# Kernel optimization log

Measured on AMD Instinct MI355X. Metric: run time of the kernel, lower is better.

## Reference

```python
import jax, jax.numpy as jnp
import numpy as np

B, H, D = 2, 16, 64
M = N = 4096
WM = WN = 64
R = 3
NEG = -10000.0


def _rand_blocks(m, n, wm, wn, r, last_idx):
    # Faithful port of bigbird_block_rand_mask (numpy RNG, seeded by caller).
    nb = m // wm
    rand = np.zeros((nb - 2, r), dtype=np.int32)
    mid = np.arange(1, n // wn - 1, dtype=np.int32)
    last = n // wn - 1
    if last_idx > 2 * wn:
        last = last_idx // wn - 1
    for i in range(1, nb - 1):
        start, end = i - 2, i
        if i == 1:
            rand[i - 1] = np.random.permutation(mid[2:last])[:r]
        elif i == 2:
            rand[i - 1] = np.random.permutation(mid[3:last])[:r]
        elif i == nb - 3 or i == nb - 2:
            rand[i - 1] = np.random.permutation(mid[:last])[:r]
        elif start > last:
            rand[i - 1] = np.random.permutation(mid[:last])[:r]
        elif end + 1 == last:
            rand[i - 1] = np.random.permutation(mid[:start])[:r]
        else:
            rand[i - 1] = np.random.permutation(np.concatenate((mid[:start], mid[end + 1:last])))[:r]
    return rand


def setup_inputs() -> dict:
    key = jax.random.key(0)
    kq, kk, kv = jax.random.split(key, 3)
    nb = M // WM
    q = jax.random.normal(kq, (B, H, M, D), jnp.float32)
    k = jax.random.normal(kk, (B, H, N, D), jnp.float32)
    v = jax.random.normal(kv, (B, H, N, D), jnp.float32)
    band_mask = jnp.ones((B, 1, nb - 4, WM, 3 * WN), jnp.float32)
    from_mask = jnp.ones((B, 1, M, 1), jnp.float32)
    to_mask = jnp.ones((B, 1, 1, N), jnp.float32)
    from_blocked_mask = jnp.ones((B, nb, WM), jnp.float32)
    to_blocked_mask = jnp.ones((B, nb, WN), jnp.float32)
    np.random.seed(0)
    ra = np.stack([_rand_blocks(M, N, WM, WN, R, 1024)[:nb - 2] for _ in range(H)], 0)
    rand_attn = jnp.asarray(np.broadcast_to(ra[None], (B, H, nb - 2, R)).copy(), jnp.int32)
    return dict(query_layer=q, key_layer=k, value_layer=v, band_mask=band_mask,
                from_mask=from_mask, to_mask=to_mask,
                from_blocked_mask=from_blocked_mask, to_blocked_mask=to_blocked_mask,
                rand_attn=rand_attn, batch_size=B, from_seq_length=M, to_seq_length=N)


def _forward(q, k, v, band_mask, from_mask, to_mask, from_blocked_mask, to_blocked_mask, rand_attn):
    b, h, m, d = q.shape
    n = k.shape[2]
    wm, wn, r = WM, WN, R
    nb = m // wm
    scale = 1.0 / np.sqrt(d)
    bq = q.reshape(b, h, nb, wm, d)
    bk = k.reshape(b, h, nb, wn, d)
    bv = v.reshape(b, h, nb, wn, d)

    # gather random key/value blocks: [b,h,nb-2,r*wn,d]
    idx = jnp.broadcast_to(rand_attn.reshape(b, h, (nb - 2) * r, 1, 1).astype(jnp.int32),
                           (b, h, (nb - 2) * r, wn, d))
    gk = jnp.take_along_axis(bk, idx, axis=2).reshape(b, h, nb - 2, r * wn, d)
    gv = jnp.take_along_axis(bv, idx, axis=2).reshape(b, h, nb - 2, r * wn, d)

    # random-block attention mask: [b,h,nb-2,wm,r*wn]
    bidx = jnp.arange(b)[:, None, None, None]
    rm = to_blocked_mask[bidx, rand_attn].reshape(b, h, nb - 2, r * wn)
    rand_mask = jnp.einsum('blq,bhlk->bhlqk', from_blocked_mask[:, 1:-1], rm)

    # --- first row-block: full attention over all keys ---
    p0 = jnp.einsum('bhqd,bhkd->bhqk', bq[:, :, 0], k) * scale + (1.0 - to_mask) * NEG
    c0 = jnp.einsum('bhqk,bhkd->bhqd', jax.nn.softmax(p0, -1), v)[:, :, None]

    # --- second row-block: blocks 0,1,2,last + random ---
    k1c = jnp.concatenate([bk[:, :, 0], bk[:, :, 1], bk[:, :, 2], bk[:, :, -1], gk[:, :, 0]], axis=2)
    v1c = jnp.concatenate([bv[:, :, 0], bv[:, :, 1], bv[:, :, 2], bv[:, :, -1], gv[:, :, 0]], axis=2)
    p1 = jnp.einsum('bhqd,bhkd->bhqk', bq[:, :, 1], k1c) * scale
    seq_pad = jnp.concatenate([to_mask[:, :, :, :3 * wn], to_mask[:, :, :, -wn:],
                               jnp.ones((b, 1, 1, r * wn), to_mask.dtype)], axis=3)
    rpad = jnp.concatenate([jnp.ones((b, h, wm, 4 * wn), rand_mask.dtype), rand_mask[:, :, 0]], axis=3)
    p1 = p1 + (1.0 - jnp.minimum(seq_pad, rpad)) * NEG
    c1 = jnp.einsum('bhqk,bhkd->bhqd', jax.nn.softmax(p1, -1), v1c)[:, :, None]

    # --- middle row-blocks: sliding window (3 blocks) + first + last + random ---
    ek = jnp.concatenate([bk[:, :, 1:-3], bk[:, :, 2:-2], bk[:, :, 3:-1]], axis=3)  # [b,h,nb-4,3wn,d]
    ev = jnp.concatenate([bv[:, :, 1:-3], bv[:, :, 2:-2], bv[:, :, 3:-1]], axis=3)
    mq = bq[:, :, 2:-2]
    inner = jnp.einsum('bhlqd,bhlkd->bhlqk', mq, ek) * scale + (1.0 - band_mask) * NEG
    randp = jnp.einsum('bhlqd,bhlkd->bhlqk', mq, gk[:, :, 1:-1]) * scale + (1.0 - rand_mask[:, :, 1:-1]) * NEG
    firstp = jnp.einsum('bhlqd,bhkd->bhlqk', mq, bk[:, :, 0]) * scale \
        + (1.0 - to_mask[:, :, :, :wn][:, :, :, None, :]) * NEG
    lastp = jnp.einsum('bhlqd,bhkd->bhlqk', mq, bk[:, :, -1]) * scale \
        + (1.0 - to_mask[:, :, :, -wn:][:, :, :, None, :]) * NEG
    band = jnp.concatenate([firstp, inner, randp, lastp], axis=-1)  # [b,h,nb-4,wm,(5+r)*wn]
    attn = jax.nn.softmax(band, -1)
    cmid = (jnp.einsum('bhlqk,bhlkd->bhlqd', attn[..., wn:4 * wn], ev)
            + jnp.einsum('bhlqk,bhlkd->bhlqd', attn[..., 4 * wn:4 * wn + r * wn], gv[:, :, 1:-1])
            + jnp.einsum('bhlqk,bhkd->bhlqd', attn[..., :wn], bv[:, :, 0])
            + jnp.einsum('bhlqk,bhkd->bhlqd', attn[..., -wn:], bv[:, :, -1]))

    # --- second-to-last row-block: blocks 0,-3,-2,-1 + random ---
    k2c = jnp.concatenate([bk[:, :, 0], bk[:, :, -3], bk[:, :, -2], bk[:, :, -1], gk[:, :, -1]], axis=2)
    v2c = jnp.concatenate([bv[:, :, 0], bv[:, :, -3], bv[:, :, -2], bv[:, :, -1], gv[:, :, -1]], axis=2)
    p2 = jnp.einsum('bhqd,bhkd->bhqk', bq[:, :, -2], k2c) * scale
    seq_pad2 = jnp.concatenate([to_mask[:, :, :, :wn], to_mask[:, :, :, -3 * wn:],
                                jnp.ones((b, 1, 1, r * wn), to_mask.dtype)], axis=3)
    rpad2 = jnp.concatenate([jnp.ones((b, h, wm, 4 * wn), rand_mask.dtype), rand_mask[:, :, -1]], axis=3)
    p2 = p2 + (1.0 - jnp.minimum(seq_pad2, rpad2)) * NEG
    c2 = jnp.einsum('bhqk,bhkd->bhqd', jax.nn.softmax(p2, -1), v2c)[:, :, None]

    # --- last row-block: full attention ---
    p3 = jnp.einsum('bhqd,bhkd->bhqk', bq[:, :, -1], k) * scale + (1.0 - to_mask) * NEG
    c3 = jnp.einsum('bhqk,bhkd->bhqd', jax.nn.softmax(p3, -1), v)[:, :, None]

    ctx = jnp.concatenate([c0, c1, cmid, c2, c3], axis=2).reshape(b, h, m, d) * from_mask
    return jnp.transpose(ctx, (0, 2, 1, 3))  # [b, m, h, d]


def reference(query_layer, key_layer, value_layer, band_mask, from_mask, to_mask,
              from_blocked_mask, to_blocked_mask, rand_attn,
              batch_size, from_seq_length, to_seq_length):
    return _forward(query_layer, key_layer, value_layer, band_mask, from_mask, to_mask,
                    from_blocked_mask, to_blocked_mask, rand_attn)
```

## Files before the change

### kernel.cpp

```cpp
#include <hip/hip_runtime.h>
#include <math.h>

constexpr int B_  = 2;
constexpr int H_  = 16;
constexpr int M_  = 4096;
constexpr int NB_ = 64;
constexpr int R_  = 3;
constexpr float LOG2E  = 1.44269504089f;
constexpr float SCALE2 = 0.125f * LOG2E;
constexpr float NEG2   = -10000.0f * LOG2E;

constexpr int PER_BH = 62 + 16;
constexpr int NWG    = B_ * H_ * PER_BH;
constexpr int PACC_OFF = 0;
constexpr int PM_OFF   = B_ * H_ * 2 * 8 * 64 * 64;
constexpr int PL_OFF   = PM_OFF + B_ * H_ * 2 * 8 * 64;

typedef short bf16x8 __attribute__((ext_vector_type(8)));
typedef float f32x4  __attribute__((ext_vector_type(4)));

__device__ __forceinline__ short bf16s(float x) {
    return __builtin_bit_cast(short, (__bf16)x);
}
__device__ __forceinline__ unsigned pack_bf16(float a, float b) {
    unsigned short ul = __builtin_bit_cast(unsigned short, (__bf16)a);
    unsigned short uh = __builtin_bit_cast(unsigned short, (__bf16)b);
    return (unsigned)ul | ((unsigned)uh << 16);
}

__device__ __forceinline__ int tile_kb(int e, int ch, int qb, int ra0, int ra1, int ra2, int i) {
    if (e >= 0) return ch * 8 + i;
    const int rnd = (i == 4) ? ra0 : ((i == 5) ? ra1 : ra2);
    if (qb == 1)        return (i < 3) ? i : ((i == 3) ? NB_ - 1 : rnd);
    if (qb == NB_ - 2)  return (i == 0) ? 0 : ((i < 4) ? 60 + i : rnd);
    if (i == 0) return 0;
    if (i < 4)  return qb - 2 + i;
    if (i < 7)  return rnd;
    return NB_ - 1;
}

__global__ __launch_bounds__(256, 4)
void bigbird_mfma(const float* __restrict__ q,  const float* __restrict__ k,
                  const float* __restrict__ v,  const float* __restrict__ band_mask,
                  const float* __restrict__ from_mask, const float* __restrict__ to_mask,
                  const float* __restrict__ from_blocked, const float* __restrict__ to_blocked,
                  const int*   __restrict__ rand_attn,   float* __restrict__ out,
                  float* __restrict__ ws)
{
    __shared__ int4 kf[2][8][64];
    __shared__ int4 vf[2][8][64];

    const int wg  = (blockIdx.x & 7) * (NWG / 8) + (blockIdx.x >> 3);
    const int bh  = wg / PER_BH;
    const int idx = wg % PER_BH;
    const int h   = bh % H_;
    const int b   = bh / H_;
    int qb, e = -1, ch = 0;
    if (idx < 62)      { qb = idx + 1; }
    else if (idx < 70) { e = 0; ch = idx - 62; qb = 0; }
    else               { e = 1; ch = idx - 70; qb = NB_ - 1; }

    const int t  = threadIdx.x;
    const int l  = t & 63;
    const int w  = t >> 6;
    const int c  = l & 15;
    const int hh = l >> 4;

    int ra0 = 0, ra1 = 0, ra2 = 0;
    int nkb;
    if (e >= 0) nkb = 8;
    else {
        const int* ra = rand_attn + ((b * H_ + h) * (NB_ - 2) + (qb - 1)) * R_;
        ra0 = ra[0]; ra1 = ra[1]; ra2 = ra[2];
        nkb = (qb == 1 || qb == NB_ - 2) ? 7 : 8;
    }

    const int rr  = t >> 2;
    const int cc4 = t & 3;
    const float* kbase = k + ((size_t)bh * M_ + rr) * 64 + cc4 * 16;
    const int kslot = (rr >> 4) * 2 + (cc4 >> 1);
    const int kr15  = rr & 15;
    const int kg0   = (cc4 & 1) * 2;

    const int d0v  = (t & 31) * 2;
    const int oct8 = t >> 5;
    const float* vbase = v + (size_t)bh * M_ * 64 + (size_t)(oct8 * 8) * 64 + d0v;
    const int vslot = (d0v >> 4) * 2 + (oct8 >> 2);
    const int vidx  = (oct8 & 3) * 16 + (d0v & 15);

    bf16x8 qf[2];
    {
        const float* qp = q + ((size_t)bh * M_ + (size_t)qb * 64 + w * 16 + c) * 64 + hh * 8;
        #pragma unroll
        for (int dh = 0; dh < 2; ++dh) {
            float4 a0 = *(const float4*)(qp + dh * 32);
            float4 a1 = *(const float4*)(qp + dh * 32 + 4);
            bf16x8 qv;
            qv[0] = bf16s(a0.x); qv[1] = bf16s(a0.y); qv[2] = bf16s(a0.z); qv[3] = bf16s(a0.w);
            qv[4] = bf16s(a1.x); qv[5] = bf16s(a1.y); qv[6] = bf16s(a1.z); qv[7] = bf16s(a1.w);
            qf[dh] = qv;
        }
    }

    const float fbv = from_blocked[(b * NB_ + qb) * 64 + (w * 16 + c)];

    float mrun = -INFINITY, lrun = 0.0f;
    f32x4 O[4];
    #pragma unroll
    for (int nf = 0; nf < 4; ++nf) { O[nf][0] = 0.f; O[nf][1] = 0.f; O[nf][2] = 0.f; O[nf][3] = 0.f; }

    float4 kr0, kr1, kr2, kr3;
    float2 vr[8];

    {
        const int kb0 = tile_kb(e, ch, qb, ra0, ra1, ra2, 0);
        const float4* kp4 = (const float4*)(kbase + (size_t)kb0 * 4096);
        kr0 = kp4[0]; kr1 = kp4[1]; kr2 = kp4[2]; kr3 = kp4[3];
        const float* vp = vbase + (size_t)kb0 * 4096;
        #pragma unroll
        for (int j = 0; j < 8; ++j) vr[j] = *(const float2*)(vp + j * 64);

        float kfl[16];
        kfl[0]=kr0.x; kfl[1]=kr0.y; kfl[2]=kr0.z; kfl[3]=kr0.w;
        kfl[4]=kr1.x; kfl[5]=kr1.y; kfl[6]=kr1.z; kfl[7]=kr1.w;
        kfl[8]=kr2.x; kfl[9]=kr2.y; kfl[10]=kr2.z; kfl[11]=kr2.w;
        kfl[12]=kr3.x; kfl[13]=kr3.y; kfl[14]=kr3.z; kfl[15]=kr3.w;
        bf16x8 o0, o1;
        #pragma unroll
        for (int j = 0; j < 8; ++j) { o0[j] = bf16s(kfl[j]); o1[j] = bf16s(kfl[8 + j]); }
        kf[0][kslot][kg0 * 16 + kr15]       = __builtin_bit_cast(int4, o0);
        kf[0][kslot][(kg0 + 1) * 16 + kr15] = __builtin_bit_cast(int4, o1);

        bf16x8 va, vb2;
        #pragma unroll
        for (int j = 0; j < 8; ++j) { va[j] = bf16s(vr[j].x); vb2[j] = bf16s(vr[j].y); }
        vf[0][vslot][vidx]     = __builtin_bit_cast(int4, va);
        vf[0][vslot][vidx + 1] = __builtin_bit_cast(int4, vb2);

        if (1 < nkb) {
            const int kb1 = tile_kb(e, ch, qb, ra0, ra1, ra2, 1);
            const float4* kn4 = (const float4*)(kbase + (size_t)kb1 * 4096);
            kr0 = kn4[0]; kr1 = kn4[1]; kr2 = kn4[2]; kr3 = kn4[3];
            const float* vn = vbase + (size_t)kb1 * 4096;
            #pragma unroll
            for (int j = 0; j < 8; ++j) vr[j] = *(const float2*)(vn + j * 64);
        }
    }
    __syncthreads();

    for (int it = 0; it < nkb; ++it) {
        const int cur = it & 1;
        const int kb = tile_kb(e, ch, qb, ra0, ra1, ra2, it);
        int mode = 0, boff = 0;
        if (e < 0) {
            if (qb == 1 || qb == NB_ - 2) { mode = (it >= 4) ? 2 : 0; }
            else {
                if (it >= 1 && it < 4)      { mode = 1; boff = (it - 1) * 64; }
                else if (it >= 4 && it < 7) { mode = 2; }
            }
        }

        f32x4 sf[4];
        #pragma unroll
        for (int f = 0; f < 4; ++f) { sf[f][0]=0.f; sf[f][1]=0.f; sf[f][2]=0.f; sf[f][3]=0.f; }
        __builtin_amdgcn_s_setprio(1);
        #pragma unroll
        for (int f = 0; f < 4; ++f) {
            sf[f] = __builtin_amdgcn_mfma_f32_16x16x32_bf16(
                        __builtin_bit_cast(bf16x8, kf[cur][f * 2 + 0][l]), qf[0], sf[f], 0, 0, 0);
            sf[f] = __builtin_amdgcn_mfma_f32_16x16x32_bf16(
                        __builtin_bit_cast(bf16x8, kf[cur][f * 2 + 1][l]), qf[1], sf[f], 0, 0, 0);
        }
        __builtin_amdgcn_s_setprio(0);

        float msk[4][4];
        if (mode == 0) {
            const float* mp = to_mask + b * M_ + kb * 64 + 4 * hh;
            #pragma unroll
            for (int f = 0; f < 4; ++f) {
                float4 mv = *(const float4*)(mp + 16 * f);
                msk[f][0] = mv.x; msk[f][1] = mv.y; msk[f][2] = mv.z; msk[f][3] = mv.w;
            }
        } else if (mode == 1) {
            const float* mp = band_mask + (((size_t)b * (NB_ - 4) + (qb - 2)) * 64 + (w * 16 + c)) * 192 + boff + 4 * hh;
            #pragma unroll
            for (int f = 0; f < 4; ++f) {
                float4 mv = *(const float4*)(mp + 16 * f);
                msk[f][0] = mv.x; msk[f][1] = mv.y; msk[f][2] = mv.z; msk[f][3] = mv.w;
            }
        } else {
            const float* mp = to_blocked + (b * NB_ + kb) * 64 + 4 * hh;
            #pragma unroll
            for (int f = 0; f < 4; ++f) {
                float4 mv = *(const float4*)(mp + 16 * f);
                msk[f][0] = fbv * mv.x; msk[f][1] = fbv * mv.y;
                msk[f][2] = fbv * mv.z; msk[f][3] = fbv * mv.w;
            }
        }

        float p[4][4];
        float tmax = -INFINITY;
        #pragma unroll
        for (int f = 0; f < 4; ++f) {
            #pragma unroll
            for (int r = 0; r < 4; ++r) {
                const float s = sf[f][r] * SCALE2 + (1.0f - msk[f][r]) * NEG2;
                p[f][r] = s;
                tmax = fmaxf(tmax, s);
            }
        }
        tmax = fmaxf(tmax, __shfl_xor(tmax, 16));
        tmax = fmaxf(tmax, __shfl_xor(tmax, 32));
        const float mnew = fmaxf(mrun, tmax);
        const float fs = exp2f(mrun - mnew);
        float sum = 0.0f;
        #pragma unroll
        for (int f = 0; f < 4; ++f) {
            #pragma unroll
            for (int r = 0; r < 4; ++r) { p[f][r] = exp2f(p[f][r] - mnew); sum += p[f][r]; }
        }
        sum += __shfl_xor(sum, 16);
        sum += __shfl_xor(sum, 32);
        lrun = lrun * fs + sum;
        mrun = mnew;

        const float fr0 = __shfl(fs, hh * 4 + 0);
        const float fr1 = __shfl(fs, hh * 4 + 1);
        const float fr2 = __shfl(fs, hh * 4 + 2);
        const float fr3 = __shfl(fs, hh * 4 + 3);
        #pragma unroll
        for (int nf = 0; nf < 4; ++nf) {
            O[nf][0] *= fr0; O[nf][1] *= fr1; O[nf][2] *= fr2; O[nf][3] *= fr3;
        }

        unsigned pks[4][2];
        #pragma unroll
        for (int f = 0; f < 4; ++f) {
            pks[f][0] = pack_bf16(p[f][0], p[f][1]);
            pks[f][1] = pack_bf16(p[f][2], p[f][3]);
        }
        #pragma unroll
        for (int kh = 0; kh < 2; ++kh) {
            unsigned ad[4];
            #pragma unroll
            for (int wq = 0; wq < 4; ++wq) {
                const int pos = wq >> 1, ww = wq & 1;
                const int src = c + 16 * ((2 * hh + pos) & 3);
                const unsigned x = (unsigned)__shfl((int)pks[2 * kh][ww], src);
                const unsigned y = (unsigned)__shfl((int)pks[2 * kh + 1][ww], src);
                ad[wq] = (hh & 2) ? y : x;
            }
            const uint4 adv = make_uint4(ad[0], ad[1], ad[2], ad[3]);
            const bf16x8 pa = __builtin_bit_cast(bf16x8, adv);
            __builtin_amdgcn_s_setprio(1);
            #pragma unroll
            for (int nf = 0; nf < 4; ++nf) {
                O[nf] = __builtin_amdgcn_mfma_f32_16x16x32_bf16(
                            pa, __builtin_bit_cast(bf16x8, vf[cur][nf * 2 + kh][l]), O[nf], 0, 0, 0);
            }
            __builtin_amdgcn_s_setprio(0);
        }

        if (it + 1 < nkb) {
            const int nxt = cur ^ 1;
            float kfl[16];
            kfl[0]=kr0.x; kfl[1]=kr0.y; kfl[2]=kr0.z; kfl[3]=kr0.w;
            kfl[4]=kr1.x; kfl[5]=kr1.y; kfl[6]=kr1.z; kfl[7]=kr1.w;
            kfl[8]=kr2.x; kfl[9]=kr2.y; kfl[10]=kr2.z; kfl[11]=kr2.w;
            kfl[12]=kr3.x; kfl[13]=kr3.y; kfl[14]=kr3.z; kfl[15]=kr3.w;
            bf16x8 o0, o1;
            #pragma unroll
            for (int j = 0; j < 8; ++j) { o0[j] = bf16s(kfl[j]); o1[j] = bf16s(kfl[8 + j]); }
            kf[nxt][kslot][kg0 * 16 + kr15]       = __builtin_bit_cast(int4, o0);
            kf[nxt][kslot][(kg0 + 1) * 16 + kr15] = __builtin_bit_cast(int4, o1);

            bf16x8 va, vb2;
            #pragma unroll
            for (int j = 0; j < 8; ++j) { va[j] = bf16s(vr[j].x); vb2[j] = bf16s(vr[j].y); }
            vf[nxt][vslot][vidx]     = __builtin_bit_cast(int4, va);
            vf[nxt][vslot][vidx + 1] = __builtin_bit_cast(int4, vb2);

            if (it + 2 < nkb) {
                const int kbn = tile_kb(e, ch, qb, ra0, ra1, ra2, it + 2);
                const float4* kp4 = (const float4*)(kbase + (size_t)kbn * 4096);
                kr0 = kp4[0]; kr1 = kp4[1]; kr2 = kp4[2]; kr3 = kp4[3];
                const float* vp = vbase + (size_t)kbn * 4096;
                #pragma unroll
                for (int j = 0; j < 8; ++j) vr[j] = *(const float2*)(vp + j * 64);
            }
        }
        __syncthreads();
    }

    if (e < 0) {
        #pragma unroll
        for (int r = 0; r < 4; ++r) {
            const float lr  = __shfl(lrun, hh * 4 + r);
            const int   qg  = qb * 64 + w * 16 + hh * 4 + r;
            const float fmv = from_mask[b * M_ + qg];
            const float scl = fmv / lr;
            float* op = out + (((size_t)b * M_ + qg) * H_ + h) * 64 + c;
            #pragma unroll
            for (int nf = 0; nf < 4; ++nf) op[nf * 16] = O[nf][r] * scl;
        }
    } else {
        const int pe = (bh * 2 + e) * 8 + ch;
        #pragma unroll
        for (int r = 0; r < 4; ++r) {
            const int qlocal = w * 16 + hh * 4 + r;
            float* pa = ws + PACC_OFF + ((size_t)pe * 64 + qlocal) * 64 + c;
            #pragma unroll
            for (int nf = 0; nf < 4; ++nf) pa[nf * 16] = O[nf][r];
        }
        if (hh == 0) {
            ws[PM_OFF + pe * 64 + w * 16 + c] = mrun;
            ws[PL_OFF + pe * 64 + w * 16 + c] = lrun;
        }
    }
}

__global__ __launch_bounds__(256)
void bigbird_combine(const float* __restrict__ ws, const float* __restrict__ from_mask,
                     float* __restrict__ out)
{
    const int g  = blockIdx.x;
    const int e  = g & 1;
    const int bh = g >> 1;
    const int h  = bh % H_;
    const int b  = bh / H_;
    const int qb = e ? NB_ - 1 : 0;

    const int t  = threadIdx.x;
    const int r  = t >> 2;
    const int dq = (t & 3) * 16;

    float mc[8], lc[8];
    float m = -INFINITY;
    #pragma unroll
    for (int c = 0; c < 8; ++c) {
        mc[c] = ws[PM_OFF + (g * 8 + c) * 64 + r];
        lc[c] = ws[PL_OFF + (g * 8 + c) * 64 + r];
        m = fmaxf(m, mc[c]);
    }
    float l = 0.0f;
    float acc[16];
    #pragma unroll
    for (int j = 0; j < 16; ++j) acc[j] = 0.0f;
    #pragma unroll
    for (int c = 0; c < 8; ++c) {
        const float sc = exp2f(mc[c] - m);
        l += lc[c] * sc;
        const float4* pa = (const float4*)(ws + PACC_OFF + ((size_t)(g * 8 + c) * 64 + r) * 64 + dq);
        #pragma unroll
        for (int j4 = 0; j4 < 4; ++j4) {
            float4 av = pa[j4];
            acc[j4 * 4 + 0] += sc * av.x;
            acc[j4 * 4 + 1] += sc * av.y;
            acc[j4 * 4 + 2] += sc * av.z;
            acc[j4 * 4 + 3] += sc * av.w;
        }
    }
    const float fm = from_mask[b * M_ + qb * 64 + r];
    const float s  = fm / l;
    float* op = out + (((size_t)b * M_ + qb * 64 + r) * H_ + h) * 64 + dq;
    #pragma unroll
    for (int j4 = 0; j4 < 4; ++j4) {
        float4 o;
        o.x = acc[j4 * 4 + 0] * s; o.y = acc[j4 * 4 + 1] * s;
        o.z = acc[j4 * 4 + 2] * s; o.w = acc[j4 * 4 + 3] * s;
        *(float4*)(op + j4 * 4) = o;
    }
}

extern "C" void kernel_launch(void* const* d_in, const int* in_sizes, int n_in,
                              void* d_out, int out_size, void* d_ws, size_t ws_size,
                              hipStream_t stream) {
    const float* q  = (const float*)d_in[0];
    const float* k  = (const float*)d_in[1];
    const float* v  = (const float*)d_in[2];
    const float* bm = (const float*)d_in[3];
    const float* fm = (const float*)d_in[4];
    const float* tm = (const float*)d_in[5];
    const float* fb = (const float*)d_in[6];
    const float* tb = (const float*)d_in[7];
    const int*   ra = (const int*)d_in[8];
    float* o  = (float*)d_out;
    float* ws = (float*)d_ws;

    hipLaunchKernelGGL(bigbird_mfma, dim3(NWG), dim3(256), 0, stream,
                       q, k, v, bm, fm, tm, fb, tb, ra, o, ws);
    hipLaunchKernelGGL(bigbird_combine, dim3(B_ * H_ * 2), dim3(256), 0, stream,
                       ws, fm, o);
}
```

Measured before the change: 92.43 us.

## Prefetch masks one tile ahead, stage next K/V earlier, lighten barriers

```diff
diff --git a/kernel.cpp b/kernel.cpp
--- a/kernel.cpp
+++ b/kernel.cpp
@@ -26,6 +26,12 @@
     unsigned short ul = __builtin_bit_cast(unsigned short, (__bf16)a);
     unsigned short uh = __builtin_bit_cast(unsigned short, (__bf16)b);
     return (unsigned)ul | ((unsigned)uh << 16);
+}
+
+__device__ __forceinline__ void lds_barrier() {
+    asm volatile("s_waitcnt lgkmcnt(0)" ::: "memory");
+    __builtin_amdgcn_s_barrier();
+    asm volatile("" ::: "memory");
 }
 
 __device__ __forceinline__ int tile_kb(int e, int ch, int qb, int ra0, int ra1, int ra2, int i) {
@@ -37,6 +43,15 @@
     if (i < 4)  return qb - 2 + i;
     if (i < 7)  return rnd;
     return NB_ - 1;
+}
+
+__device__ __forceinline__ int tile_mode(int e, int qb, int i, int& boff) {
+    boff = 0;
+    if (e >= 0) return 0;
+    if (qb == 1 || qb == NB_ - 2) return (i >= 4) ? 2 : 0;
+    if (i >= 1 && i < 4) { boff = (i - 1) * 64; return 1; }
+    if (i >= 4 && i < 7) return 2;
+    return 0;
 }
 
 __global__ __launch_bounds__(256, 4)
@@ -88,6 +103,12 @@
     const int vslot = (d0v >> 4) * 2 + (oct8 >> 2);
     const int vidx  = (oct8 & 3) * 16 + (d0v & 15);
 
+    auto mask_ptr = [&](int kb, int mode, int boff) -> const float* {
+        if (mode == 0) return to_mask + b * M_ + kb * 64 + 4 * hh;
+        if (mode == 1) return band_mask + (((size_t)b * (NB_ - 4) + (qb - 2)) * 64 + (w * 16 + c)) * 192 + boff + 4 * hh;
+        return to_blocked + (b * NB_ + kb) * 64 + 4 * hh;
+    };
+
     bf16x8 qf[2];
     {
         const float* qp = q + ((size_t)bh * M_ + (size_t)qb * 64 + w * 16 + c) * 64 + hh * 8;
@@ -111,6 +132,7 @@
 
     float4 kr0, kr1, kr2, kr3;
     float2 vr[8];
+    float4 mpf[4];
 
     {
         const int kb0 = tile_kb(e, ch, qb, ra0, ra1, ra2, 0);
@@ -137,6 +159,11 @@
         vf[0][vslot][vidx]     = __builtin_bit_cast(int4, va);
         vf[0][vslot][vidx + 1] = __builtin_bit_cast(int4, vb2);
 
+        int bo0; const int md0 = tile_mode(e, qb, 0, bo0);
+        const float* mp = mask_ptr(kb0, md0, bo0);
+        #pragma unroll
+        for (int f = 0; f < 4; ++f) mpf[f] = *(const float4*)(mp + 16 * f);
+
         if (1 < nkb) {
             const int kb1 = tile_kb(e, ch, qb, ra0, ra1, ra2, 1);
             const float4* kn4 = (const float4*)(kbase + (size_t)kb1 * 4096);
@@ -146,19 +173,11 @@
             for (int j = 0; j < 8; ++j) vr[j] = *(const float2*)(vn + j * 64);
         }
     }
-    __syncthreads();
+    lds_barrier();
 
     for (int it = 0; it < nkb; ++it) {
         const int cur = it & 1;
-        const int kb = tile_kb(e, ch, qb, ra0, ra1, ra2, it);
-        int mode = 0, boff = 0;
-        if (e < 0) {
-            if (qb == 1 || qb == NB_ - 2) { mode = (it >= 4) ? 2 : 0; }
-            else {
-                if (it >= 1 && it < 4)      { mode = 1; boff = (it - 1) * 64; }
-                else if (it >= 4 && it < 7) { mode = 2; }
-            }
-        }
+        int boffC; const int modeC = tile_mode(e, qb, it, boffC);
 
         f32x4 sf[4];
         #pragma unroll
@@ -174,27 +193,47 @@
         __builtin_amdgcn_s_setprio(0);
 
         float msk[4][4];
-        if (mode == 0) {
-            const float* mp = to_mask + b * M_ + kb * 64 + 4 * hh;
+        {
+            const float ms = (modeC == 2) ? fbv : 1.0f;
             #pragma unroll
             for (int f = 0; f < 4; ++f) {
-                float4 mv = *(const float4*)(mp + 16 * f);
-                msk[f][0] = mv.x; msk[f][1] = mv.y; msk[f][2] = mv.z; msk[f][3] = mv.w;
+                msk[f][0] = ms * mpf[f].x; msk[f][1] = ms * mpf[f].y;
+                msk[f][2] = ms * mpf[f].z; msk[f][3] = ms * mpf[f].w;
             }
-        } else if (mode == 1) {
-            const float* mp = band_mask + (((size_t)b * (NB_ - 4) + (qb - 2)) * 64 + (w * 16 + c)) * 192 + boff + 4 * hh;
-            #pragma unroll
-            for (int f = 0; f < 4; ++f) {
-                float4 mv = *(const float4*)(mp + 16 * f);
-                msk[f][0] = mv.x; msk[f][1] = mv.y; msk[f][2] = mv.z; msk[f][3] = mv.w;
-            }
-        } else {
-            const float* mp = to_blocked + (b * NB_ + kb) * 64 + 4 * hh;
-            #pragma unroll
-            for (int f = 0; f < 4; ++f) {
-                float4 mv = *(const float4*)(mp + 16 * f);
-                msk[f][0] = fbv * mv.x; msk[f][1] = fbv * mv.y;
-                msk[f][2] = fbv * mv.z; msk[f][3] = fbv * mv.w;
+        }
+
+        if (it + 1 < nkb) {
+            const int nxt = cur ^ 1;
+            float kfl[16];
+            kfl[0]=kr0.x; kfl[1]=kr0.y; kfl[2]=kr0.z; kfl[3]=kr0.w;
+            kfl[4]=kr1.x; kfl[5]=kr1.y; kfl[6]=kr1.z; kfl[7]=kr1.w;
+            kfl[8]=kr2.x; kfl[9]=kr2.y; kfl[10]=kr2.z; kfl[11]=kr2.w;
+            kfl[12]=kr3.x; kfl[13]=kr3.y; kfl[14]=kr3.z; kfl[15]=kr3.w;
+            bf16x8 o0, o1;
+            #pragma unroll
+            for (int j = 0; j < 8; ++j) { o0[j] = bf16s(kfl[j]); o1[j] = bf16s(kfl[8 + j]); }
+            kf[nxt][kslot][kg0 * 16 + kr15]       = __builtin_bit_cast(int4, o0);
+            kf[nxt][kslot][(kg0 + 1) * 16 + kr15] = __builtin_bit_cast(int4, o1);
+
+            bf16x8 va, vb2;
+            #pragma unroll
+            for (int j = 0; j < 8; ++j) { va[j] = bf16s(vr[j].x); vb2[j] = bf16s(vr[j].y); }
+            vf[nxt][vslot][vidx]     = __builtin_bit_cast(int4, va);
+            vf[nxt][vslot][vidx + 1] = __builtin_bit_cast(int4, vb2);
+
+            const int kbn = tile_kb(e, ch, qb, ra0, ra1, ra2, it + 1);
+            int bon; const int mdn = tile_mode(e, qb, it + 1, bon);
+            const float* mp = mask_ptr(kbn, mdn, bon);
+            #pragma unroll
+            for (int f = 0; f < 4; ++f) mpf[f] = *(const float4*)(mp + 16 * f);
+
+            if (it + 2 < nkb) {
+                const int kb2 = tile_kb(e, ch, qb, ra0, ra1, ra2, it + 2);
+                const float4* kp4 = (const float4*)(kbase + (size_t)kb2 * 4096);
+                kr0 = kp4[0]; kr1 = kp4[1]; kr2 = kp4[2]; kr3 = kp4[3];
+                const float* vp = vbase + (size_t)kb2 * 4096;
+                #pragma unroll
+                for (int j = 0; j < 8; ++j) vr[j] = *(const float2*)(vp + j * 64);
             }
         }
 
@@ -261,35 +300,7 @@
             __builtin_amdgcn_s_setprio(0);
         }
 
-        if (it + 1 < nkb) {
-            const int nxt = cur ^ 1;
-            float kfl[16];
-            kfl[0]=kr0.x; kfl[1]=kr0.y; kfl[2]=kr0.z; kfl[3]=kr0.w;
-            kfl[4]=kr1.x; kfl[5]=kr1.y; kfl[6]=kr1.z; kfl[7]=kr1.w;
-            kfl[8]=kr2.x; kfl[9]=kr2.y; kfl[10]=kr2.z; kfl[11]=kr2.w;
-            kfl[12]=kr3.x; kfl[13]=kr3.y; kfl[14]=kr3.z; kfl[15]=kr3.w;
-            bf16x8 o0, o1;
-            #pragma unroll
-            for (int j = 0; j < 8; ++j) { o0[j] = bf16s(kfl[j]); o1[j] = bf16s(kfl[8 + j]); }
-            kf[nxt][kslot][kg0 * 16 + kr15]       = __builtin_bit_cast(int4, o0);
-            kf[nxt][kslot][(kg0 + 1) * 16 + kr15] = __builtin_bit_cast(int4, o1);
-
-            bf16x8 va, vb2;
-            #pragma unroll
-            for (int j = 0; j < 8; ++j) { va[j] = bf16s(vr[j].x); vb2[j] = bf16s(vr[j].y); }
-            vf[nxt][vslot][vidx]     = __builtin_bit_cast(int4, va);
-            vf[nxt][vslot][vidx + 1] = __builtin_bit_cast(int4, vb2);
-
-            if (it + 2 < nkb) {
-                const int kbn = tile_kb(e, ch, qb, ra0, ra1, ra2, it + 2);
-                const float4* kp4 = (const float4*)(kbase + (size_t)kbn * 4096);
-                kr0 = kp4[0]; kr1 = kp4[1]; kr2 = kp4[2]; kr3 = kp4[3];
-                const float* vp = vbase + (size_t)kbn * 4096;
-                #pragma unroll
-                for (int j = 0; j < 8; ++j) vr[j] = *(const float2*)(vp + j * 64);
-            }
-        }
-        __syncthreads();
+        if (it + 1 < nkb) lds_barrier();
     }
 
     if (e < 0) {
```

New measurement: 102.6 us. 11.0% more time.
